# Performance work log

Hardware: AMD Instinct MI355X
Metric: run time of the kernel (lower is better)

The kernel has to match this reference:

```python
import jax, jax.numpy as jnp
import numpy as np

# --- fixed model configuration (from init_kwargs) ---
NX, NY, NU, NP = 8, 8, 2, 5
DELTA = 0.01
PHO, CP, AR, AB = 5.0, 6.0, 3.0, 3.0
KR, KB, TD, QR, QB = 2.5, 1.5, 300.0, 200.0, 200.0
CAF, TF = 6.0, 320.0
YMEAN = jnp.array([50.0, 1.0, 0.5, 313.0, 50.0, 1.0, 0.5, 313.0], jnp.float32)
YSTD = jnp.array([2.0, 0.2, 0.1, 4.0, 2.0, 0.2, 0.1, 4.0], jnp.float32)
UMEAN = jnp.array([10.0, 5.0], jnp.float32)
USTD = jnp.array([1.0, 0.5], jnp.float32)


def _fg(x, u):
    """Grey-box CSTR+flash ODE RHS. x: [B,8] scaled, u: [B,2] scaled."""
    x = x * YSTD + YMEAN
    u = u * USTD + UMEAN
    Hr, CAr, CBr, Tr = x[..., 0:1], x[..., 1:2], x[..., 2:3], x[..., 3:4]
    Hb, CAb, CBb, Tb = x[..., 4:5], x[..., 5:6], x[..., 6:7], x[..., 7:8]
    F, D = u[..., 0:1], u[..., 1:2]
    Fr = KR * jnp.sqrt(Hr)
    Fb = KB * jnp.sqrt(Hb)
    dHr = (F + D - Fr) / AR
    dCAr = (F * (CAF - CAr) - D * CAr) / (AR * Hr)
    dCBr = (-F * CBr - D * CBr) / (AR * Hr)
    dTr = (F * (TF - Tr) + D * (TD - Tr)) / (AR * Hr) + QR / (PHO * AR * CP * Hr)
    dHb = (Fr - Fb - D) / AB
    dCAb = (Fr * (CAr - CAb) + D * CAb) / (AB * Hb)
    dCBb = (Fr * (CBr - CBb) + D * CBb) / (AB * Hb)
    dTb = Fr * (Tr - Tb) / (AB * Hb) + QB / (PHO * AB * CP * Hb)
    xdot = jnp.concatenate([dHr, dCAr, dCBr, dTr, dHb, dCAb, dCBb, dTb], axis=-1)
    return xdot / YSTD


def setup_inputs() -> dict:
    key = jax.random.key(0)
    ks = jax.random.split(key, 6)
    B, T = 2048, 128
    d_in, d_h = NX + NP * (NY + NU) + NU, 128  # 60, 128
    useq = jax.random.normal(ks[0], (B, T, NU), jnp.float32)
    xGz0 = jax.random.normal(ks[1], (B, NX + NP * (NY + NU)), jnp.float32)
    W1 = jax.random.normal(ks[2], (d_in, d_h), jnp.float32) * (1.0 / np.sqrt(d_in))
    b1 = jnp.zeros((d_h,), jnp.float32)
    W2 = jax.random.normal(ks[3], (d_h, d_h), jnp.float32) * (1.0 / np.sqrt(d_h))
    b2 = jnp.zeros((d_h,), jnp.float32)
    W3 = jax.random.normal(ks[4], (d_h, NX), jnp.float32) * (1.0 / np.sqrt(d_h))
    b3 = jnp.zeros((NX,), jnp.float32)
    return {"useq": useq, "xGz0": xGz0, "W1": W1, "b1": b1,
            "W2": W2, "b2": b2, "W3": W3, "b3": b3}


def reference(useq, xGz0, W1, b1, W2, b2, W3, b3):
    def fnn(inp):
        h = jnp.tanh(inp @ W1 + b1)
        h = jnp.tanh(h @ W2 + b2)
        return h @ W3 + b3

    def interp(yfull):  # [B,(Np+1)*Ny] -> [B,Np*Ny]
        B = yfull.shape[0]
        y = yfull.reshape(B, NP + 1, NY)
        return (0.5 * (y[:, :-1] + y[:, 1:])).reshape(B, NP * NY)

    def step(xGz, u):
        xG = xGz[:, :NX]
        z = xGz[:, NX:]
        ypseq = z[:, :NP * NY]
        upseq = z[:, NP * NY:]
        # k1
        k1 = _fg(xG, u) + fnn(jnp.concatenate((xG, z, u), axis=-1))
        # interpolated half-step past sequence
        yp_interp = interp(jnp.concatenate((ypseq, xG), axis=-1))
        z_half = jnp.concatenate((yp_interp, upseq), axis=-1)
        x2 = xG + DELTA * (k1 / 2)
        k2 = _fg(x2, u) + fnn(jnp.concatenate((x2, z_half, u), axis=-1))
        x3 = xG + DELTA * (k2 / 2)
        k3 = _fg(x3, u) + fnn(jnp.concatenate((x3, z_half, u), axis=-1))
        yp_shift = jnp.concatenate((ypseq[:, NY:], xG), axis=-1)
        z_full = jnp.concatenate((yp_shift, upseq), axis=-1)
        x4 = xG + DELTA * k3
        k4 = _fg(x4, u) + fnn(jnp.concatenate((x4, z_full, u), axis=-1))
        y = xG
        xGplus = xG + (DELTA / 6) * (k1 + 2 * k2 + 2 * k3 + k4)
        zplus = jnp.concatenate((yp_shift, upseq[:, NU:], u), axis=-1)
        return jnp.concatenate((xGplus, zplus), axis=-1), y

    u_t = jnp.swapaxes(useq, 0, 1)  # [T,B,Nu]
    _, ys = jax.lax.scan(step, xGz0, u_t)  # ys: [T,B,Ny]
    return jnp.swapaxes(ys, 0, 1)  # [B,T,Ny]
```

## Files before the change

### kernel.cpp

```cpp
#include <hip/hip_runtime.h>
#include <math.h>

#define BLOCK 512
#define ROWS 8

typedef __attribute__((ext_vector_type(8))) short s16x8;
typedef __attribute__((ext_vector_type(4))) float f32x4;

static constexpr int O_H1   = 0;
static constexpr int O_SU   = 1088;
static constexpr int O_PP   = 3168;
static constexpr int O_PRIV = 3680;
static constexpr int PRIV_DW = 640;
static constexpr int LDSN   = O_PRIV + 8 * PRIV_DW;

__device__ __forceinline__ unsigned short f2bf(float f) {
  unsigned u = __float_as_uint(f);
  return (unsigned short)((u + 0x7fffu + ((u >> 16) & 1u)) >> 16);
}
__device__ __forceinline__ unsigned cvt_pk_bf16(float lo, float hi) {
  unsigned r;
  asm("v_cvt_pk_bf16_f32 %0, %1, %2" : "=v"(r) : "v"(lo), "v"(hi));
  return r;
}
__device__ __forceinline__ float tanh_fast(float x) {
  float e = __builtin_amdgcn_exp2f(x * 2.88539008177792681f);
  return fmaf(-2.f, __builtin_amdgcn_rcpf(e + 1.f), 1.f);
}

#define MFMA16(A, B, C) __builtin_amdgcn_mfma_f32_16x16x32_bf16((A), (B), (C), 0, 0, 0)

extern "C" __global__ void __launch_bounds__(BLOCK, 1)
cstr_rk4_mfma8(const float* __restrict__ useq, const float* __restrict__ xGz0,
               const float* __restrict__ W1, const float* __restrict__ b1,
               const float* __restrict__ W2, const float* __restrict__ b2,
               const float* __restrict__ W3, const float* __restrict__ b3,
               float* __restrict__ out)
{
  extern __shared__ float smf[];
  unsigned short* h1h = (unsigned short*)(smf + O_H1);
  unsigned*       h1u = (unsigned*)(smf + O_H1);
  float* su = smf + O_SU;
  float* pp = smf + O_PP;

  const int tid  = threadIdx.x;
  const int w    = tid >> 6;
  const int l    = tid & 63;
  const int nn   = l & 15;
  const int hh   = l >> 4;
  const int r    = l >> 3;
  const int c    = l & 7;
  const int base = blockIdx.x * ROWS;

  float* wp_ = smf + O_PRIV + w * PRIV_DW;
  unsigned short* inhp = (unsigned short*)wp_;
  float* xmp = wp_ + 576;

  for (int i = tid; i < 8 * 260; i += BLOCK) {
    int row = i / 260, col = i % 260;
    su[i] = (col < 256) ? useq[(size_t)base * 256 + row * 256 + col] : 0.f;
  }
  for (int i = l; i < 16 * 72; i += 64) {
    int n_ = i / 72, k = i % 72;
    unsigned short v = 0;
    if (n_ < ROWS) {
      if (k < 58)      v = f2bf(xGz0[(size_t)(base + n_) * 58 + k]);
      else if (k < 60) v = f2bf(useq[(size_t)(base + n_) * 256 + (k - 58)]);
    }
    inhp[i] = v;
  }
  xmp[l] = xGz0[(size_t)(base + r) * 58 + c];

  const size_t rowb = (size_t)(base + r) * 58;
  float xg  = xGz0[rowb + c];
  float yp0 = xGz0[rowb + 8 + c],  yp1 = xGz0[rowb + 16 + c];
  float yp2 = xGz0[rowb + 24 + c], yp3 = xGz0[rowb + 32 + c];
  float yp4 = xGz0[rowb + 40 + c];
  float upA = xGz0[rowb + 48 + c];
  float upB = (c < 2) ? xGz0[rowb + 56 + c] : 0.f;
  float b3r = b3[c];
  float kacc = 0.f;

  const int j = 16 * w + nn;
  s16x8 a10, a11, a20, a21, a22, a23, a3h;
  #pragma unroll
  for (int i = 0; i < 8; ++i) {
    int k0 = 8 * hh + i, k1 = 32 + 8 * hh + i;
    a10[i] = (short)f2bf(W1[k0 * 128 + j]);
    a11[i] = (short)((k1 < 60) ? f2bf(W1[k1 * 128 + j]) : 0);
    a20[i] = (short)f2bf(W2[(     8 * hh + i) * 128 + j]);
    a21[i] = (short)f2bf(W2[(32 + 8 * hh + i) * 128 + j]);
    a22[i] = (short)f2bf(W2[(64 + 8 * hh + i) * 128 + j]);
    a23[i] = (short)f2bf(W2[(96 + 8 * hh + i) * 128 + j]);
    unsigned short z = 0;
    if (i < 4 && nn < 8) z = f2bf(W3[(16 * w + 4 * hh + i) * 8 + nn]);
    a3h[i] = (short)z;
  }
  const float4 bva = *(const float4*)(b1 + 16 * w + 4 * hh);
  const float4 bvb = *(const float4*)(b2 + 16 * w + 4 * hh);

  __syncthreads();

  #pragma unroll 1
  for (int t = 0; t < 128; ++t) {
    const float u0r = su[r * 260 + 2 * t];
    const float u1r = su[r * 260 + 2 * t + 1];
    if (w == 0) out[((size_t)(base + r) * 128 + t) * 8 + c] = xg;

    #pragma unroll
    for (int s = 0; s < 4; ++s) {
      {
        s16x8 bb0 = *(const s16x8*)(inhp + nn * 72 + 8 * hh);
        s16x8 bb1 = *(const s16x8*)(inhp + nn * 72 + 32 + 8 * hh);
        f32x4 c1 = (f32x4){0.f, 0.f, 0.f, 0.f};
        c1 = MFMA16(a10, bb0, c1);
        c1 = MFMA16(a11, bb1, c1);
        float t0 = tanh_fast(c1[0] + bva.x);
        float t1 = tanh_fast(c1[1] + bva.y);
        float t2 = tanh_fast(c1[2] + bva.z);
        float t3 = tanh_fast(c1[3] + bva.w);
        uint2 pk; pk.x = cvt_pk_bf16(t0, t1); pk.y = cvt_pk_bf16(t2, t3);
        *(uint2*)(h1u + nn * 68 + 8 * w + 2 * hh) = pk;
      }
      __syncthreads();

      {
        const unsigned short* h1row = h1h + nn * 136;
        s16x8 q0 = *(const s16x8*)(h1row +  0 + 8 * hh);
        s16x8 q1 = *(const s16x8*)(h1row + 32 + 8 * hh);
        s16x8 q2 = *(const s16x8*)(h1row + 64 + 8 * hh);
        s16x8 q3 = *(const s16x8*)(h1row + 96 + 8 * hh);
        f32x4 c2 = (f32x4){0.f, 0.f, 0.f, 0.f};
        c2 = MFMA16(a20, q0, c2); c2 = MFMA16(a21, q1, c2);
        c2 = MFMA16(a22, q2, c2); c2 = MFMA16(a23, q3, c2);
        float t0 = tanh_fast(c2[0] + bvb.x);
        float t1 = tanh_fast(c2[1] + bvb.y);
        float t2 = tanh_fast(c2[2] + bvb.z);
        float t3 = tanh_fast(c2[3] + bvb.w);
        s16x8 bf3;
        ((unsigned*)&bf3)[0] = cvt_pk_bf16(t0, t1);
        ((unsigned*)&bf3)[1] = cvt_pk_bf16(t2, t3);
        ((unsigned*)&bf3)[2] = 0u;
        ((unsigned*)&bf3)[3] = 0u;
        f32x4 c3p = (f32x4){0.f, 0.f, 0.f, 0.f};
        c3p = MFMA16(a3h, bf3, c3p);
        if (nn < 8 && hh < 2)
          *(float4*)(pp + w * 64 + nn * 8 + 4 * hh) =
              make_float4(c3p[0], c3p[1], c3p[2], c3p[3]);
      }
      __syncthreads();

      {
        float nv = b3r;
        #pragma unroll
        for (int ww = 0; ww < 8; ++ww) nv += pp[ww * 64 + l];
        float4 xa = *(const float4*)(xmp + r * 8);
        float4 xb = *(const float4*)(xmp + r * 8 + 4);
        float Hr  = fmaf(xa.x, 2.f, 50.f),  CAr = fmaf(xa.y, 0.2f, 1.f);
        float CBr = fmaf(xa.z, 0.1f, 0.5f), Tr  = fmaf(xa.w, 4.f, 313.f);
        float Hb  = fmaf(xb.x, 2.f, 50.f),  CAb = fmaf(xb.y, 0.2f, 1.f);
        float CBb = fmaf(xb.z, 0.1f, 0.5f), Tb  = fmaf(xb.w, 4.f, 313.f);
        float F = u0r + 10.f, D = fmaf(u1r, 0.5f, 5.f);
        float Fr = 2.5f * sqrtf(Hr), Fb = 1.5f * sqrtf(Hb);
        float rH = __builtin_amdgcn_rcpf(3.f * Hr);
        float rB = __builtin_amdgcn_rcpf(3.f * Hb);
        float k0 = (F + D - Fr) * (1.f / 6.f);
        float k1 = (F * (6.f - CAr) - D * CAr) * (5.f * rH);
        float k2 = (-(F + D) * CBr) * (10.f * rH);
        float k3 = (F * (320.f - Tr) + D * (300.f - Tr)) * (0.25f * rH) + (5.f / 3.f) * rH;
        float k4 = (Fr - Fb - D) * (1.f / 6.f);
        float k5 = (Fr * (CAr - CAb) + D * CAb) * (5.f * rB);
        float k6 = (Fr * (CBr - CBb) + D * CBb) * (10.f * rB);
        float k7 = Fr * (Tr - Tb) * (0.25f * rB) + (5.f / 3.f) * rB;
        float fgc = (c & 4) ? ((c & 2) ? ((c & 1) ? k7 : k6) : ((c & 1) ? k5 : k4))
                            : ((c & 2) ? ((c & 1) ? k3 : k2) : ((c & 1) ? k1 : k0));
        float kv = fgc + nv;
        float cc;
        if (s == 0)      { kacc = kv;                  cc = fmaf(kv, 0.005f, xg); }
        else if (s == 1) { kacc = fmaf(kv, 2.f, kacc); cc = fmaf(kv, 0.005f, xg); }
        else if (s == 2) { kacc = fmaf(kv, 2.f, kacc); cc = fmaf(kv, 0.01f,  xg); }
        else             { xg = fmaf(kacc + kv, 0.01f / 6.f, xg); cc = xg; }
        xmp[r * 8 + c] = cc;
        inhp[r * 72 + c] = f2bf(cc);

        if (s == 0) {
          inhp[r * 72 +  8 + c] = f2bf(0.5f * (yp0 + yp1));
          inhp[r * 72 + 16 + c] = f2bf(0.5f * (yp1 + yp2));
          inhp[r * 72 + 24 + c] = f2bf(0.5f * (yp2 + yp3));
          inhp[r * 72 + 32 + c] = f2bf(0.5f * (yp3 + yp4));
          inhp[r * 72 + 40 + c] = f2bf(0.5f * (yp4 + xg));
        } else if (s == 2) {
          inhp[r * 72 +  8 + c] = f2bf(yp1);
          inhp[r * 72 + 16 + c] = f2bf(yp2);
          inhp[r * 72 + 24 + c] = f2bf(yp3);
          inhp[r * 72 + 32 + c] = f2bf(yp4);
          inhp[r * 72 + 40 + c] = f2bf(xg);
          yp0 = yp1; yp1 = yp2; yp2 = yp3; yp3 = yp4; yp4 = xg;
        } else if (s == 3) {
          float tA = __shfl(upA, r * 8 + ((c + 2) & 7));
          float tB = __shfl(upB, r * 8 + ((c >= 6) ? (c - 6) : 0));
          float nu = (c < 6) ? tA : tB;
          upA = nu;
          inhp[r * 72 + 48 + c] = f2bf(nu);
          if (c < 2) {
            float uv = (c == 0) ? u0r : u1r;
            upB = uv;
            inhp[r * 72 + 56 + c] = f2bf(uv);
            if (t < 127)
              inhp[r * 72 + 58 + c] = f2bf(su[r * 260 + 2 * (t + 1) + c]);
          }
        }
      }
    }
  }
}

extern "C" void kernel_launch(void* const* d_in, const int* in_sizes, int n_in,
                              void* d_out, int out_size, void* d_ws, size_t ws_size,
                              hipStream_t stream) {
  const float* useq = (const float*)d_in[0];
  const float* xGz0 = (const float*)d_in[1];
  const float* W1   = (const float*)d_in[2];
  const float* b1   = (const float*)d_in[3];
  const float* W2   = (const float*)d_in[4];
  const float* b2   = (const float*)d_in[5];
  const float* W3   = (const float*)d_in[6];
  const float* b3   = (const float*)d_in[7];
  float* out = (float*)d_out;

  size_t lds = (size_t)LDSN * sizeof(float);
  (void)hipFuncSetAttribute((const void*)cstr_rk4_mfma8,
                            hipFuncAttributeMaxDynamicSharedMemorySize, (int)lds);
  hipLaunchKernelGGL(cstr_rk4_mfma8, dim3(2048 / ROWS), dim3(BLOCK), lds, stream,
                     useq, xGz0, W1, b1, W2, b2, W3, b3, out);
}
```

Before: 482.7 us.

## Halve rows per block to double grid size and raise occupancy

Each block now handles 4 batch rows instead of 8, so the grid has 512 blocks instead of 256, and launch bounds allow up to 4 blocks per CU. The serial time-step chain is latency-bound, and more resident blocks are meant to hide barrier and MFMA latency. The MFMA tiles stay 16 wide, so half the lanes compute duplicated rows that are masked off before stores, which doubles the total MFMA work. It also switches the scalar bf16 conversion to the hardware pack instruction.

```diff
diff --git a/kernel.cpp b/kernel.cpp
--- a/kernel.cpp
+++ b/kernel.cpp
@@ -2,15 +2,15 @@
 #include <math.h>
 
 #define BLOCK 512
-#define ROWS 8
+#define ROWS 4
 
 typedef __attribute__((ext_vector_type(8))) short s16x8;
 typedef __attribute__((ext_vector_type(4))) float f32x4;
 
 static constexpr int O_H1   = 0;
 static constexpr int O_SU   = 1088;
-static constexpr int O_PP   = 3168;
-static constexpr int O_PRIV = 3680;
+static constexpr int O_PP   = 2128;
+static constexpr int O_PRIV = 2640;
 static constexpr int PRIV_DW = 640;
 static constexpr int LDSN   = O_PRIV + 8 * PRIV_DW;
 
@@ -23,6 +23,9 @@
   asm("v_cvt_pk_bf16_f32 %0, %1, %2" : "=v"(r) : "v"(lo), "v"(hi));
   return r;
 }
+__device__ __forceinline__ unsigned short bf1(float v) {
+  return (unsigned short)cvt_pk_bf16(v, v);
+}
 __device__ __forceinline__ float tanh_fast(float x) {
   float e = __builtin_amdgcn_exp2f(x * 2.88539008177792681f);
   return fmaf(-2.f, __builtin_amdgcn_rcpf(e + 1.f), 1.f);
@@ -30,8 +33,8 @@
 
 #define MFMA16(A, B, C) __builtin_amdgcn_mfma_f32_16x16x32_bf16((A), (B), (C), 0, 0, 0)
 
-extern "C" __global__ void __launch_bounds__(BLOCK, 1)
-cstr_rk4_mfma8(const float* __restrict__ useq, const float* __restrict__ xGz0,
+extern "C" __global__ void __launch_bounds__(BLOCK, 4)
+cstr_rk4_mfma9(const float* __restrict__ useq, const float* __restrict__ xGz0,
                const float* __restrict__ W1, const float* __restrict__ b1,
                const float* __restrict__ W2, const float* __restrict__ b2,
                const float* __restrict__ W3, const float* __restrict__ b3,
@@ -50,13 +53,15 @@
   const int hh   = l >> 4;
   const int r    = l >> 3;
   const int c    = l & 7;
+  const int rs   = r & (ROWS - 1);
+  const bool st  = (r < ROWS);
   const int base = blockIdx.x * ROWS;
 
   float* wp_ = smf + O_PRIV + w * PRIV_DW;
   unsigned short* inhp = (unsigned short*)wp_;
   float* xmp = wp_ + 576;
 
-  for (int i = tid; i < 8 * 260; i += BLOCK) {
+  for (int i = tid; i < ROWS * 260; i += BLOCK) {
     int row = i / 260, col = i % 260;
     su[i] = (col < 256) ? useq[(size_t)base * 256 + row * 256 + col] : 0.f;
   }
@@ -69,9 +74,9 @@
     }
     inhp[i] = v;
   }
-  xmp[l] = xGz0[(size_t)(base + r) * 58 + c];
-
-  const size_t rowb = (size_t)(base + r) * 58;
+  xmp[l] = xGz0[(size_t)(base + rs) * 58 + c];
+
+  const size_t rowb = (size_t)(base + rs) * 58;
   float xg  = xGz0[rowb + c];
   float yp0 = xGz0[rowb + 8 + c],  yp1 = xGz0[rowb + 16 + c];
   float yp2 = xGz0[rowb + 24 + c], yp3 = xGz0[rowb + 32 + c];
@@ -103,9 +108,9 @@
 
   #pragma unroll 1
   for (int t = 0; t < 128; ++t) {
-    const float u0r = su[r * 260 + 2 * t];
-    const float u1r = su[r * 260 + 2 * t + 1];
-    if (w == 0) out[((size_t)(base + r) * 128 + t) * 8 + c] = xg;
+    const float u0r = su[rs * 260 + 2 * t];
+    const float u1r = su[rs * 260 + 2 * t + 1];
+    if (w == 0 && st) out[((size_t)(base + r) * 128 + t) * 8 + c] = xg;
 
     #pragma unroll
     for (int s = 0; s < 4; ++s) {
@@ -144,7 +149,7 @@
         ((unsigned*)&bf3)[3] = 0u;
         f32x4 c3p = (f32x4){0.f, 0.f, 0.f, 0.f};
         c3p = MFMA16(a3h, bf3, c3p);
-        if (nn < 8 && hh < 2)
+        if (nn < ROWS && hh < 2)
           *(float4*)(pp + w * 64 + nn * 8 + 4 * hh) =
               make_float4(c3p[0], c3p[1], c3p[2], c3p[3]);
       }
@@ -152,10 +157,13 @@
 
       {
         float nv = b3r;
-        #pragma unroll
-        for (int ww = 0; ww < 8; ++ww) nv += pp[ww * 64 + l];
-        float4 xa = *(const float4*)(xmp + r * 8);
-        float4 xb = *(const float4*)(xmp + r * 8 + 4);
+        {
+          const int li = rs * 8 + c;
+          #pragma unroll
+          for (int ww = 0; ww < 8; ++ww) nv += pp[ww * 64 + li];
+        }
+        float4 xa = *(const float4*)(xmp + rs * 8);
+        float4 xb = *(const float4*)(xmp + rs * 8 + 4);
         float Hr  = fmaf(xa.x, 2.f, 50.f),  CAr = fmaf(xa.y, 0.2f, 1.f);
         float CBr = fmaf(xa.z, 0.1f, 0.5f), Tr  = fmaf(xa.w, 4.f, 313.f);
         float Hb  = fmaf(xb.x, 2.f, 50.f),  CAb = fmaf(xb.y, 0.2f, 1.f);
@@ -180,35 +188,41 @@
         else if (s == 1) { kacc = fmaf(kv, 2.f, kacc); cc = fmaf(kv, 0.005f, xg); }
         else if (s == 2) { kacc = fmaf(kv, 2.f, kacc); cc = fmaf(kv, 0.01f,  xg); }
         else             { xg = fmaf(kacc + kv, 0.01f / 6.f, xg); cc = xg; }
-        xmp[r * 8 + c] = cc;
-        inhp[r * 72 + c] = f2bf(cc);
-
-        if (s == 0) {
-          inhp[r * 72 +  8 + c] = f2bf(0.5f * (yp0 + yp1));
-          inhp[r * 72 + 16 + c] = f2bf(0.5f * (yp1 + yp2));
-          inhp[r * 72 + 24 + c] = f2bf(0.5f * (yp2 + yp3));
-          inhp[r * 72 + 32 + c] = f2bf(0.5f * (yp3 + yp4));
-          inhp[r * 72 + 40 + c] = f2bf(0.5f * (yp4 + xg));
-        } else if (s == 2) {
-          inhp[r * 72 +  8 + c] = f2bf(yp1);
-          inhp[r * 72 + 16 + c] = f2bf(yp2);
-          inhp[r * 72 + 24 + c] = f2bf(yp3);
-          inhp[r * 72 + 32 + c] = f2bf(yp4);
-          inhp[r * 72 + 40 + c] = f2bf(xg);
-          yp0 = yp1; yp1 = yp2; yp2 = yp3; yp3 = yp4; yp4 = xg;
-        } else if (s == 3) {
-          float tA = __shfl(upA, r * 8 + ((c + 2) & 7));
-          float tB = __shfl(upB, r * 8 + ((c >= 6) ? (c - 6) : 0));
+
+        if (st) {
+          xmp[r * 8 + c] = cc;
+          inhp[r * 72 + c] = bf1(cc);
+
+          if (s == 0) {
+            inhp[r * 72 +  8 + c] = bf1(0.5f * (yp0 + yp1));
+            inhp[r * 72 + 16 + c] = bf1(0.5f * (yp1 + yp2));
+            inhp[r * 72 + 24 + c] = bf1(0.5f * (yp2 + yp3));
+            inhp[r * 72 + 32 + c] = bf1(0.5f * (yp3 + yp4));
+            inhp[r * 72 + 40 + c] = bf1(0.5f * (yp4 + xg));
+          } else if (s == 2) {
+            inhp[r * 72 +  8 + c] = bf1(yp1);
+            inhp[r * 72 + 16 + c] = bf1(yp2);
+            inhp[r * 72 + 24 + c] = bf1(yp3);
+            inhp[r * 72 + 32 + c] = bf1(yp4);
+            inhp[r * 72 + 40 + c] = bf1(xg);
+          }
+        }
+        if (s == 2) { yp0 = yp1; yp1 = yp2; yp2 = yp3; yp3 = yp4; yp4 = xg; }
+        else if (s == 3) {
+          float tA = __shfl(upA, (l & 56) + ((c + 2) & 7));
+          float tB = __shfl(upB, (l & 56) + ((c >= 6) ? (c - 6) : 0));
           float nu = (c < 6) ? tA : tB;
           upA = nu;
-          inhp[r * 72 + 48 + c] = f2bf(nu);
-          if (c < 2) {
-            float uv = (c == 0) ? u0r : u1r;
-            upB = uv;
-            inhp[r * 72 + 56 + c] = f2bf(uv);
-            if (t < 127)
-              inhp[r * 72 + 58 + c] = f2bf(su[r * 260 + 2 * (t + 1) + c]);
-          }
+          if (st) {
+            inhp[r * 72 + 48 + c] = bf1(nu);
+            if (c < 2) {
+              float uv = (c == 0) ? u0r : u1r;
+              upB = uv;
+              inhp[r * 72 + 56 + c] = bf1(uv);
+              if (t < 127)
+                inhp[r * 72 + 58 + c] = bf1(su[r * 260 + 2 * (t + 1) + c]);
+            }
+          } else if (c < 2) upB = (c == 0) ? u0r : u1r;
         }
       }
     }
@@ -229,8 +243,8 @@
   float* out = (float*)d_out;
 
   size_t lds = (size_t)LDSN * sizeof(float);
-  (void)hipFuncSetAttribute((const void*)cstr_rk4_mfma8,
+  (void)hipFuncSetAttribute((const void*)cstr_rk4_mfma9,
                             hipFuncAttributeMaxDynamicSharedMemorySize, (int)lds);
-  hipLaunchKernelGGL(cstr_rk4_mfma8, dim3(2048 / ROWS), dim3(BLOCK), lds, stream,
+  hipLaunchKernelGGL(cstr_rk4_mfma9, dim3(2048 / ROWS), dim3(BLOCK), lds, stream,
                      useq, xGz0, W1, b1, W2, b2, W3, b3, out);
 }
```

New measurement: 749.1 us. 1.55x slower.
